# Performance work log

Measured on AMD Instinct MI355X. Metric: run time of the kernel, lower is better.

Reference implementation:

```python
import jax, jax.numpy as jnp
import numpy as np
from jax.scipy.special import logsumexp

TAG_NAMES = ['<pad>', 'O', 'B-PER', 'I-PER', 'B-LOC', 'I-LOC', 'B-ORG', 'I-ORG', 'B-MISC', 'I-MISC']
K = len(TAG_NAMES)
T, B, D = 512, 64, 1024
PAD = 0
IMP = -100.0
VOCAB = 30000


def _crf_params(rng):
    # torchcrf reset_parameters: uniform(-0.1, 0.1), then init_crf_transitions overrides
    start = rng.uniform(-0.1, 0.1, K).astype(np.float32)
    end = rng.uniform(-0.1, 0.1, K).astype(np.float32)
    trans = rng.uniform(-0.1, 0.1, (K, K)).astype(np.float32)
    for i, name in enumerate(TAG_NAMES):
        if name[0] in ('I', 'L') or name == '<pad>':
            start[i] = IMP
        if name[0] in ('B', 'I'):
            end[i] = IMP
    tag_is = {p: [i for i, t in enumerate(TAG_NAMES) if t[0] == p] for p in 'BIOUL'}
    tag_is['P'] = [i for i, t in enumerate(TAG_NAMES) if t == 'tag']
    for ft, tos in {'B': 'BOUP', 'I': 'BOUP', 'O': 'IL', 'U': 'IL'}.items():
        for fi in tag_is[ft]:
            for tt in tos:
                for ti in tag_is[tt]:
                    trans[fi, ti] = IMP
    for ft, tos in {'B': 'IL', 'I': 'IL'}.items():
        for fi in tag_is[ft]:
            for tt in tos:
                for ti in tag_is[tt]:
                    if TAG_NAMES[fi].split('-')[1] != TAG_NAMES[ti].split('-')[1]:
                        trans[fi, ti] = IMP
    return jnp.asarray(start), jnp.asarray(end), jnp.asarray(trans)


def setup_inputs() -> dict:
    rng = np.random.default_rng(0)
    # torchcrf requires mask[0] == 1 everywhere and contiguous masks -> build from lengths
    lengths = rng.integers(T // 2, T + 1, size=B)
    valid = np.arange(T)[:, None] < lengths[None, :]  # (T, B)
    words = np.where(valid, rng.integers(1, VOCAB, size=(T, B)), PAD).astype(np.int64)
    tags = rng.integers(0, K, size=(T, B)).astype(np.int64)
    word_features = rng.standard_normal((T, B, D)).astype(np.float32)
    W = (rng.standard_normal((D, K)) / np.sqrt(D)).astype(np.float32)
    b = np.zeros(K, np.float32)
    start, end, trans = _crf_params(rng)
    return dict(words=jnp.asarray(words), tags=jnp.asarray(tags),
                word_features=jnp.asarray(word_features), W=jnp.asarray(W), b=jnp.asarray(b),
                start_trans=start, end_trans=end, transitions=trans)


def _crf_loss(emissions, tags, maskf, start, end, trans):
    """-log p(tags | emissions), summed over batch (torchcrf reduction='sum')."""
    bidx = jnp.arange(emissions.shape[1])
    # gold-path score (numerator)
    score0 = start[tags[0]] + emissions[0, bidx, tags[0]]
    em_tag = jnp.take_along_axis(emissions[1:], tags[1:, :, None], axis=-1)[..., 0]  # (T-1,B)
    step = trans[tags[:-1], tags[1:]] + em_tag
    numer = score0 + jnp.sum(step * maskf[1:], axis=0)
    seq_ends = maskf.sum(0).astype(jnp.int32) - 1
    numer = numer + end[tags[seq_ends, bidx]]
    # partition function (forward algorithm, stable log-sum-exp scan)
    def fwd_step(score, xs):
        em_t, m_t = xs
        nxt = logsumexp(score[:, :, None] + trans[None] + em_t[:, None, :], axis=1)  # (B,K)
        return jnp.where(m_t[:, None] > 0, nxt, score), None
    score, _ = jax.lax.scan(fwd_step, start[None] + emissions[0], (emissions[1:], maskf[1:]))
    denom = logsumexp(score + end[None], axis=1)
    return -(numer - denom).sum()


def _crf_decode(emissions, maskf, start, end, trans):
    """Viterbi decode; returns (T,B) int32 paths, 0-padded past sequence ends."""
    bidx = jnp.arange(emissions.shape[1])
    def vit_step(score, xs):
        em_t, m_t = xs
        bcast = score[:, :, None] + trans[None] + em_t[:, None, :]  # (B, K_prev, K_cur)
        best = bcast.max(axis=1)
        idx = bcast.argmax(axis=1).astype(jnp.int32)
        return jnp.where(m_t[:, None] > 0, best, score), idx
    score, history = jax.lax.scan(vit_step, start[None] + emissions[0], (emissions[1:], maskf[1:]))
    last_tag = jnp.argmax(score + end[None], axis=1).astype(jnp.int32)  # tag at seq_end per batch
    def back_step(tag, xs):
        hist_t, m_t = xs
        prev = jnp.where(m_t > 0, hist_t[bidx, tag], tag)
        return prev, prev
    _, path_head = jax.lax.scan(back_step, last_tag, (history, maskf[1:]), reverse=True)
    paths = jnp.concatenate([path_head, last_tag[None]], axis=0)  # (T, B)
    return jnp.where(maskf > 0, paths, 0)


def reference(words, tags, word_features, W, b, start_trans, end_trans, transitions):
    # eval-mode dropout is identity; fc projects features to tag emissions
    emissions = word_features @ W + b  # (T, B, K)
    maskf = (words != PAD).astype(emissions.dtype)  # (T, B)
    paths = _crf_decode(emissions, maskf, start_trans, end_trans, transitions)
    loss = _crf_loss(emissions, tags, maskf, start_trans, end_trans, transitions)
    return paths, loss
```

## Files before the change

### kernel.cpp

```cpp
#include <hip/hip_runtime.h>
#include <hip/hip_bf16.h>

#define TT 512
#define BB 64
#define KK 10
#define DD 1024
#define CL 32
#define NC 16

typedef unsigned char uchar;
typedef short bf16x8 __attribute__((ext_vector_type(8)));
typedef float f32x4 __attribute__((ext_vector_type(4)));

__device__ __forceinline__ unsigned f2bf(float f) {
    unsigned u = __float_as_uint(f);
    return (u + 0x7FFFu + ((u >> 16) & 1u)) >> 16;
}

__device__ __forceinline__ float max10(const float* r) {
    float m0 = fmaxf(r[0], r[1]), m1 = fmaxf(r[2], r[3]);
    float m2 = fmaxf(r[4], r[5]), m3 = fmaxf(r[6], r[7]);
    float m4 = fmaxf(r[8], r[9]);
    m0 = fmaxf(m0, m1); m2 = fmaxf(m2, m3); m0 = fmaxf(m0, m2);
    return fmaxf(m0, m4);
}

__device__ __forceinline__ float lse10(const float* r) {
    const float m = max10(r);
    float s0 = __expf(r[0] - m) + __expf(r[1] - m);
    float s1 = __expf(r[2] - m) + __expf(r[3] - m);
    float s2 = __expf(r[4] - m) + __expf(r[5] - m);
    float s3 = __expf(r[6] - m) + __expf(r[7] - m);
    float s4 = __expf(r[8] - m) + __expf(r[9] - m);
    return m + __logf(((s0 + s1) + (s2 + s3)) + s4);
}

__global__ __launch_bounds__(256, 7) void k_emissions(
    const int* __restrict__ words, const float* __restrict__ wf,
    const float* __restrict__ W, const float* __restrict__ bias,
    float* __restrict__ em, int* __restrict__ lenArr, float* loss_slot) {
    __shared__ uint4 Bfrag[32 * 40 + 1];
    const int tid = threadIdx.x;

    if (blockIdx.x == 2048) {
        int* cnt = (int*)Bfrag;
        const int b = tid & 63, seg = tid >> 6;
        int c = 0;
        for (int t = seg; t < TT; t += 4) c += (words[t * BB + b] != 0) ? 1 : 0;
        cnt[seg * 64 + b] = c;
        __syncthreads();
        if (tid < 64)
            lenArr[tid] = cnt[tid] + cnt[64 + tid] + cnt[128 + tid] + cnt[192 + tid];
        if (tid == 0) *loss_slot = 0.f;
        return;
    }

    for (int idx = tid; idx < 32 * 40; idx += 256) {
        const int ks = idx / 40, rem = idx - ks * 40;
        const int kg2 = rem / 10, col = rem - kg2 * 10;
        unsigned u[4];
        #pragma unroll
        for (int p = 0; p < 4; ++p) {
            const int k0 = ks * 32 + kg2 * 8 + p * 2;
            u[p] = f2bf(W[(size_t)k0 * KK + col]) | (f2bf(W[(size_t)(k0 + 1) * KK + col]) << 16);
        }
        Bfrag[idx] = make_uint4(u[0], u[1], u[2], u[3]);
    }
    if (tid == 0) Bfrag[1280] = make_uint4(0, 0, 0, 0);
    __syncthreads();

    const int wave = tid >> 6, lane = tid & 63;
    const int arow = lane & 15;
    const int kg   = lane >> 4;
    const int row0 = blockIdx.x * 16;
    const float* ap = wf + (size_t)(row0 + arow) * DD + wave * 256 + kg * 8;

    const int bcol  = (arow < KK) ? (wave * 8 * 40 + kg * 10 + arow) : 1280;
    const int bstep = (arow < KK) ? 40 : 0;

    f32x4 acc = {0.f, 0.f, 0.f, 0.f};
    float4 fa[4], fb[4];
    #pragma unroll
    for (int p = 0; p < 4; ++p) {
        fa[p] = *reinterpret_cast<const float4*>(ap + p * 32);
        fb[p] = *reinterpret_cast<const float4*>(ap + p * 32 + 4);
    }
    #pragma unroll
    for (int s = 0; s < 8; ++s) {
        const int r = s & 3;
        bf16x8 afr;
        afr[0] = (short)f2bf(fa[r].x); afr[1] = (short)f2bf(fa[r].y);
        afr[2] = (short)f2bf(fa[r].z); afr[3] = (short)f2bf(fa[r].w);
        afr[4] = (short)f2bf(fb[r].x); afr[5] = (short)f2bf(fb[r].y);
        afr[6] = (short)f2bf(fb[r].z); afr[7] = (short)f2bf(fb[r].w);
        if (s < 4) {
            fa[r] = *reinterpret_cast<const float4*>(ap + (s + 4) * 32);
            fb[r] = *reinterpret_cast<const float4*>(ap + (s + 4) * 32 + 4);
        }
        union { uint4 u; bf16x8 v; } bu;
        bu.u = Bfrag[bcol + s * bstep];
        acc = __builtin_amdgcn_mfma_f32_16x16x32_bf16(afr, bu.v, acc, 0, 0, 0);
    }

    __syncthreads();
    f32x4* red = (f32x4*)Bfrag;
    red[wave * 64 + lane] = acc;
    __syncthreads();
    if (wave == 0 && arow < KK) {
        f32x4 sum = red[lane];
        #pragma unroll
        for (int w = 1; w < 4; ++w) {
            const f32x4 t = red[w * 64 + lane];
            sum[0] += t[0]; sum[1] += t[1]; sum[2] += t[2]; sum[3] += t[3];
        }
        const float bk = bias[arow];
        #pragma unroll
        for (int r = 0; r < 4; ++r)
            em[(size_t)(row0 + kg * 4 + r) * KK + arow] = sum[r] + bk;
    }
}

__global__ __launch_bounds__(128) void k_chunk(
    const float* __restrict__ em, const float* __restrict__ trans,
    const int* __restrict__ lenArr, float* __restrict__ Mlse, float* __restrict__ Mmax) {
    int id = blockIdx.x;
    const bool mx = id >= 1024; id &= 1023;
    const int b = id >> 4, c = id & 15;
    const int len = lenArr[b];
    const int s_lo = c * CL + 1;
    const int s_hi = min(c * CL + CL, len - 1);
    const int ns = s_hi - s_lo + 1;
    if (ns <= 0) return;

    __shared__ float Ms[KK][12];
    __shared__ float eml[CL][KK];
    const int tid = threadIdx.x;
    for (int idx = tid; idx < CL * KK; idx += 128) {
        const int sl = idx / KK, j = idx % KK;
        const int s = s_lo + sl;
        eml[sl][j] = (s <= TT - 1) ? em[((size_t)s * BB + b) * KK + j] : 0.f;
    }
    const int i = tid / KK, j = tid % KK;
    const bool act = tid < KK * KK;
    float trc[KK];
    if (act) {
        #pragma unroll
        for (int k = 0; k < KK; ++k) trc[k] = trans[k * KK + j];
    }
    __syncthreads();
    float cur = 0.f;
    if (act) { cur = trans[i * KK + j] + eml[0][j]; Ms[i][j] = cur; }
    __syncthreads();
    for (int sl = 1; sl < ns; ++sl) {
        float row[KK];
        if (act) {
            #pragma unroll
            for (int k = 0; k < KK; ++k) row[k] = Ms[i][k] + trc[k];
        }
        __syncthreads();
        if (act) {
            cur = (mx ? max10(row) : lse10(row)) + eml[sl][j];
            Ms[i][j] = cur;
        }
        __syncthreads();
    }
    if (act) {
        float* out = mx ? Mmax : Mlse;
        out[((size_t)b * NC + c) * 100 + i * KK + j] = cur;
    }
}

__global__ __launch_bounds__(1024) void k_crf(
    const int* __restrict__ tags, const float* __restrict__ em,
    const float* __restrict__ startv, const float* __restrict__ endv,
    const float* __restrict__ trans, const int* __restrict__ lenArr,
    const float* __restrict__ Mlse, const float* __restrict__ Mmax,
    int* __restrict__ paths, float* __restrict__ loss_slot) {
    const int b = blockIdx.x;
    const int tid = threadIdx.x;
    const int wv = tid >> 6, lane = tid & 63;
    const int len = lenArr[b];

    __shared__ float Ml[NC][100];
    __shared__ float Mm[NC][100];
    __shared__ float eml[NC][CL][KK];
    __shared__ float ub[NC][KK];
    __shared__ uchar hl[NC][CL * KK];
    __shared__ int   Fl[NC][KK];
    __shared__ int   vt[NC + 1];
    __shared__ float em0[KK];
    __shared__ float red[2];

    for (int idx = tid; idx < NC * 100; idx += 1024) {
        Ml[idx / 100][idx % 100] = Mlse[(size_t)b * NC * 100 + idx];
        Mm[idx / 100][idx % 100] = Mmax[(size_t)b * NC * 100 + idx];
    }
    for (int idx = tid; idx < NC * CL * KK; idx += 1024) {
        const int c = idx / (CL * KK), r = idx % (CL * KK);
        const int sl = r / KK, j = r % KK;
        const int s = c * CL + 1 + sl;
        eml[c][sl][j] = (s <= TT - 1) ? em[((size_t)s * BB + b) * KK + j] : 0.f;
    }
    if (tid < KK) em0[tid] = em[(size_t)b * KK + tid];
    __syncthreads();

    if (wv == 0) {
        float v[KK];
        #pragma unroll
        for (int i = 0; i < KK; ++i) v[i] = startv[i] + em0[i];
        for (int c = 0; c < NC; ++c) {
            if (lane < KK) ub[c][lane] = v[lane];
            const int s_hi = min(c * CL + CL, len - 1);
            if (s_hi >= c * CL + 1) {
                float nv = 0.f;
                if (lane < KK) {
                    float r[KK];
                    #pragma unroll
                    for (int k = 0; k < KK; ++k) r[k] = v[k] + Mm[c][k * KK + lane];
                    nv = max10(r);
                }
                #pragma unroll
                for (int i = 0; i < KK; ++i) v[i] = __shfl(nv, i);
            }
        }
        float best = v[0] + endv[0];
        int bi = 0;
        #pragma unroll
        for (int i = 1; i < KK; ++i) {
            const float x = v[i] + endv[i];
            if (x > best) { best = x; bi = i; }
        }
        if (lane == 0) vt[NC] = bi;
    } else if (wv == 1) {
        float v[KK];
        #pragma unroll
        for (int i = 0; i < KK; ++i) v[i] = startv[i] + em0[i];
        for (int c = 0; c < NC; ++c) {
            const int s_hi = min(c * CL + CL, len - 1);
            if (s_hi >= c * CL + 1) {
                float nv = 0.f;
                if (lane < KK) {
                    float r[KK];
                    #pragma unroll
                    for (int k = 0; k < KK; ++k) r[k] = v[k] + Ml[c][k * KK + lane];
                    nv = lse10(r);
                }
                #pragma unroll
                for (int i = 0; i < KK; ++i) v[i] = __shfl(nv, i);
            }
        }
        float r[KK];
        #pragma unroll
        for (int i = 0; i < KK; ++i) r[i] = v[i] + endv[i];
        if (lane == 0) red[0] = lse10(r);
    } else if (wv == 2) {
        float part = 0.f;
        for (int t = 1 + lane; t < len; t += 64) {
            const int tp = tags[(t - 1) * BB + b];
            const int tc = tags[t * BB + b];
            part += trans[tp * KK + tc] + eml[(t - 1) >> 5][(t - 1) & 31][tc];
        }
        #pragma unroll
        for (int off = 32; off >= 1; off >>= 1) part += __shfl_xor(part, off);
        if (lane == 0) {
            const int t0 = tags[b];
            const int te = tags[(len - 1) * BB + b];
            red[1] = part + startv[t0] + em0[t0] + endv[te];
        }
    }
    __syncthreads();

    {
        const int c = wv;
        const int s_hi = min(c * CL + CL, len - 1);
        const int ns = s_hi - (c * CL + 1) + 1;
        if (ns > 0) {
            float trc[KK];
            if (lane < KK) {
                #pragma unroll
                for (int i = 0; i < KK; ++i) trc[i] = trans[i * KK + lane];
            }
            float s[KK];
            #pragma unroll
            for (int i = 0; i < KK; ++i) s[i] = ub[c][i];
            for (int sl = 0; sl < ns; ++sl) {
                float best = s[0] + trc[0];
                int bi = 0;
                #pragma unroll
                for (int i = 1; i < KK; ++i) {
                    const float x = s[i] + trc[i];
                    if (x > best) { best = x; bi = i; }
                }
                float snew = 0.f;
                if (lane < KK) {
                    snew = best + eml[c][sl][lane];
                    hl[c][sl * KK + lane] = (uchar)bi;
                }
                #pragma unroll
                for (int i = 0; i < KK; ++i) s[i] = __shfl(snew, i);
            }
            if (lane < KK) {
                int cur = lane;
                for (int sl = ns - 1; sl >= 0; --sl) cur = hl[c][sl * KK + cur];
                Fl[c][lane] = cur;
            }
        }
    }
    __syncthreads();

    if (tid == 0) {
        int cur = vt[NC];
        for (int c = NC - 1; c >= 0; --c) {
            const int s_hi = min(c * CL + CL, len - 1);
            if (s_hi >= c * CL + 1) cur = Fl[c][cur];
            vt[c] = cur;
        }
        atomicAdd(loss_slot, red[0] - red[1]);
    }
    __syncthreads();

    const int t0 = wv * CL;
    if (lane < CL) {
        const int t = t0 + lane;
        if (t >= len) paths[t * BB + b] = 0;
    }
    if (lane == 0) {
        const int a = min(t0 + CL, len - 1);
        if (a >= t0) {
            int cur = vt[wv + 1];
            for (int t = a; t >= t0; --t) {
                if (t <= t0 + CL - 1) paths[t * BB + b] = cur;
                if (t > t0) cur = (int)hl[wv][(t - t0 - 1) * KK + cur];
            }
        }
    }
}

extern "C" void kernel_launch(void* const* d_in, const int* in_sizes, int n_in,
                              void* d_out, int out_size, void* d_ws, size_t ws_size,
                              hipStream_t stream) {
    const int*   words  = (const int*)d_in[0];
    const int*   tags   = (const int*)d_in[1];
    const float* wf     = (const float*)d_in[2];
    const float* W      = (const float*)d_in[3];
    const float* bias   = (const float*)d_in[4];
    const float* startv = (const float*)d_in[5];
    const float* endv   = (const float*)d_in[6];
    const float* trans  = (const float*)d_in[7];

    float* em   = (float*)d_ws;
    float* Mlse = em + 327680;
    float* Mmax = Mlse + 102400;
    int*   lenA = (int*)(Mmax + 102400);

    int*   paths     = (int*)d_out;
    float* loss_slot = ((float*)d_out) + TT * BB;

    k_emissions<<<2049, 256, 0, stream>>>(words, wf, W, bias, em, lenA, loss_slot);
    k_chunk<<<2048, 128, 0, stream>>>(em, trans, lenA, Mlse, Mmax);
    k_crf<<<64, 1024, 0, stream>>>(tags, em, startv, endv, trans, lenA,
                                   Mlse, Mmax, paths, loss_slot);
}
```

Baseline: 97.52 us.

## Split emission GEMM into bf16 convert pass and fragment-layout MFMA kernel

The fused emission kernel, which converted fp32 features to bf16 and ran MFMA per 16-row tile, is split in two. A convert kernel streams the features, writes bf16 data in MFMA fragment order to a 64MB workspace, and builds the W fragments once. A second kernel then loads those fragments directly and runs the MFMAs. This adds a full extra write and read of half-size feature data plus an extra launch, in exchange for simpler, fully coalesced access in each pass.

```diff
diff --git a/kernel.cpp b/kernel.cpp
--- a/kernel.cpp
+++ b/kernel.cpp
@@ -35,88 +35,94 @@
     return m + __logf(((s0 + s1) + (s2 + s3)) + s4);
 }
 
-__global__ __launch_bounds__(256, 7) void k_emissions(
+__global__ __launch_bounds__(256) void k_convert(
     const int* __restrict__ words, const float* __restrict__ wf,
-    const float* __restrict__ W, const float* __restrict__ bias,
-    float* __restrict__ em, int* __restrict__ lenArr, float* loss_slot) {
-    __shared__ uint4 Bfrag[32 * 40 + 1];
+    const float* __restrict__ W, uint4* __restrict__ frag,
+    int* __restrict__ lenArr, float* loss_slot, uint4* __restrict__ Bfg) {
     const int tid = threadIdx.x;
-
     if (blockIdx.x == 2048) {
-        int* cnt = (int*)Bfrag;
+        __shared__ int cnt[4][64];
         const int b = tid & 63, seg = tid >> 6;
         int c = 0;
         for (int t = seg; t < TT; t += 4) c += (words[t * BB + b] != 0) ? 1 : 0;
-        cnt[seg * 64 + b] = c;
+        cnt[seg][b] = c;
         __syncthreads();
         if (tid < 64)
-            lenArr[tid] = cnt[tid] + cnt[64 + tid] + cnt[128 + tid] + cnt[192 + tid];
+            lenArr[tid] = cnt[0][tid] + cnt[1][tid] + cnt[2][tid] + cnt[3][tid];
         if (tid == 0) *loss_slot = 0.f;
+        for (int idx = tid; idx < 32 * 40; idx += 256) {
+            const int ks = idx / 40, rem = idx - ks * 40;
+            const int kg = rem / 10, col = rem - kg * 10;
+            unsigned u[4];
+            #pragma unroll
+            for (int p = 0; p < 4; ++p) {
+                const int k0 = ks * 32 + kg * 8 + p * 2;
+                u[p] = f2bf(W[(size_t)k0 * KK + col]) |
+                       (f2bf(W[(size_t)(k0 + 1) * KK + col]) << 16);
+            }
+            Bfg[idx] = make_uint4(u[0], u[1], u[2], u[3]);
+        }
         return;
     }
-
-    for (int idx = tid; idx < 32 * 40; idx += 256) {
-        const int ks = idx / 40, rem = idx - ks * 40;
-        const int kg2 = rem / 10, col = rem - kg2 * 10;
-        unsigned u[4];
-        #pragma unroll
-        for (int p = 0; p < 4; ++p) {
-            const int k0 = ks * 32 + kg2 * 8 + p * 2;
-            u[p] = f2bf(W[(size_t)k0 * KK + col]) | (f2bf(W[(size_t)(k0 + 1) * KK + col]) << 16);
-        }
-        Bfrag[idx] = make_uint4(u[0], u[1], u[2], u[3]);
-    }
-    if (tid == 0) Bfrag[1280] = make_uint4(0, 0, 0, 0);
-    __syncthreads();
-
-    const int wave = tid >> 6, lane = tid & 63;
-    const int arow = lane & 15;
-    const int kg   = lane >> 4;
-    const int row0 = blockIdx.x * 16;
-    const float* ap = wf + (size_t)(row0 + arow) * DD + wave * 256 + kg * 8;
-
-    const int bcol  = (arow < KK) ? (wave * 8 * 40 + kg * 10 + arow) : 1280;
-    const int bstep = (arow < KK) ? 40 : 0;
-
+    const int t0 = blockIdx.x * 256 + tid;
+    #pragma unroll
+    for (int i = 0; i < 8; ++i) {
+        const int tt = i * 524288 + t0;
+        const size_t e = (size_t)tt * 8;
+        const float4 f0 = *reinterpret_cast<const float4*>(wf + e);
+        const float4 f1 = *reinterpret_cast<const float4*>(wf + e + 4);
+        uint4 o;
+        o.x = f2bf(f0.x) | (f2bf(f0.y) << 16);
+        o.y = f2bf(f0.z) | (f2bf(f0.w) << 16);
+        o.z = f2bf(f1.x) | (f2bf(f1.y) << 16);
+        o.w = f2bf(f1.z) | (f2bf(f1.w) << 16);
+        const int r = tt >> 7, dblk = tt & 127;
+        const int tile = r >> 4, arow = r & 15;
+        const int ks = dblk >> 2, kg = dblk & 3;
+        frag[(size_t)tile * 2048 + ks * 64 + kg * 16 + arow] = o;
+    }
+}
+
+__global__ __launch_bounds__(256) void k_mfma(
+    const uint4* __restrict__ frag, const uint4* __restrict__ Bfg,
+    const float* __restrict__ bias, float* __restrict__ em) {
+    __shared__ f32x4 red[256];
+    const int tid = threadIdx.x;
+    const int wv = tid >> 6, lane = tid & 63;
+    const int arow = lane & 15, kg = lane >> 4;
+    const int tile = blockIdx.x;
+
+    const uint4* src = frag + (size_t)tile * 2048 + wv * 8 * 64 + lane;
+    bf16x8 a[8];
+    #pragma unroll
+    for (int q = 0; q < 8; ++q) {
+        union { uint4 u; bf16x8 v; } tu; tu.u = src[q * 64]; a[q] = tu.v;
+    }
+    const int bcol = kg * 10 + (arow < KK ? arow : KK - 1);
+    bf16x8 bq[8];
+    #pragma unroll
+    for (int q = 0; q < 8; ++q) {
+        union { uint4 u; bf16x8 v; } tu; tu.u = Bfg[(wv * 8 + q) * 40 + bcol]; bq[q] = tu.v;
+    }
     f32x4 acc = {0.f, 0.f, 0.f, 0.f};
-    float4 fa[4], fb[4];
     #pragma unroll
-    for (int p = 0; p < 4; ++p) {
-        fa[p] = *reinterpret_cast<const float4*>(ap + p * 32);
-        fb[p] = *reinterpret_cast<const float4*>(ap + p * 32 + 4);
-    }
-    #pragma unroll
-    for (int s = 0; s < 8; ++s) {
-        const int r = s & 3;
-        bf16x8 afr;
-        afr[0] = (short)f2bf(fa[r].x); afr[1] = (short)f2bf(fa[r].y);
-        afr[2] = (short)f2bf(fa[r].z); afr[3] = (short)f2bf(fa[r].w);
-        afr[4] = (short)f2bf(fb[r].x); afr[5] = (short)f2bf(fb[r].y);
-        afr[6] = (short)f2bf(fb[r].z); afr[7] = (short)f2bf(fb[r].w);
-        if (s < 4) {
-            fa[r] = *reinterpret_cast<const float4*>(ap + (s + 4) * 32);
-            fb[r] = *reinterpret_cast<const float4*>(ap + (s + 4) * 32 + 4);
-        }
-        union { uint4 u; bf16x8 v; } bu;
-        bu.u = Bfrag[bcol + s * bstep];
-        acc = __builtin_amdgcn_mfma_f32_16x16x32_bf16(afr, bu.v, acc, 0, 0, 0);
-    }
-
-    __syncthreads();
-    f32x4* red = (f32x4*)Bfrag;
-    red[wave * 64 + lane] = acc;
-    __syncthreads();
-    if (wave == 0 && arow < KK) {
-        f32x4 sum = red[lane];
+    for (int q = 0; q < 8; ++q)
+        acc = __builtin_amdgcn_mfma_f32_16x16x32_bf16(a[q], bq[q], acc, 0, 0, 0);
+
+    red[tid] = acc;
+    __syncthreads();
+    if (wv == 0 && arow < KK) {
+        f32x4 s = red[lane];
         #pragma unroll
         for (int w = 1; w < 4; ++w) {
-            const f32x4 t = red[w * 64 + lane];
-            sum[0] += t[0]; sum[1] += t[1]; sum[2] += t[2]; sum[3] += t[3];
+            const f32x4 p = red[w * 64 + lane];
+            s[0] += p[0]; s[1] += p[1]; s[2] += p[2]; s[3] += p[3];
         }
         const float bk = bias[arow];
+        const int row0 = tile * 16;
         #pragma unroll
         for (int r = 0; r < 4; ++r)
-            em[(size_t)(row0 + kg * 4 + r) * KK + arow] = sum[r] + bk;
+            em[(size_t)(row0 + kg * 4 + r) * KK + arow] = s[r] + bk;
     }
 }
 
@@ -348,15 +354,19 @@
     const float* endv   = (const float*)d_in[6];
     const float* trans  = (const float*)d_in[7];
 
-    float* em   = (float*)d_ws;
-    float* Mlse = em + 327680;
-    float* Mmax = Mlse + 102400;
-    int*   lenA = (int*)(Mmax + 102400);
+    uchar* base = (uchar*)d_ws;
+    uint4* frag = (uint4*)base;
+    float* em   = (float*)(base + 67108864);
+    float* Mlse = (float*)(base + 68419584);
+    float* Mmax = (float*)(base + 68829184);
+    int*   lenA = (int*)  (base + 69238784);
+    uint4* Bfg  = (uint4*)(base + 69239040);
 
     int*   paths     = (int*)d_out;
     float* loss_slot = ((float*)d_out) + TT * BB;
 
-    k_emissions<<<2049, 256, 0, stream>>>(words, wf, W, bias, em, lenA, loss_slot);
+    k_convert<<<2049, 256, 0, stream>>>(words, wf, W, frag, lenA, loss_slot, Bfg);
+    k_mfma<<<2048, 256, 0, stream>>>(frag, Bfg, bias, em);
     k_chunk<<<2048, 128, 0, stream>>>(em, trans, lenA, Mlse, Mmax);
     k_crf<<<64, 1024, 0, stream>>>(tags, em, startv, endv, trans, lenA,
                                    Mlse, Mmax, paths, loss_slot);
```

Result: slower. 120.7 us (+23.8%).
